# Kernel optimization log

Hardware: AMD Instinct MI355X
Metric: run time of the kernel (lower is better)

Reference implementation:

```python
import jax, jax.numpy as jnp
import numpy as np

B, T, C, H = 8, 1024, 1024, 16
D = C // H
EPS = 1e-5

def _ln(x, g, b):
    mu = jnp.mean(x, axis=-1, keepdims=True)
    var = jnp.var(x, axis=-1, keepdims=True)
    return (x - mu) * jax.lax.rsqrt(var + EPS) * g + b

def _build_mask(cond_mask, cond_len, token_len):
    # Vectorized form of the per-batch Python-loop mask in the torch module.
    counts = jnp.sum(cond_mask, axis=-1)            # [B] number of valid cond tokens
    rows = jnp.arange(T)
    cols = jnp.arange(T)
    # all rows may attend to the first counts[i] (cond) columns
    m_cond = cols[None, None, :] < counts[:, None, None]          # [B,1,T]
    m_cond = jnp.broadcast_to(m_cond, (B, T, T))
    # block-causal tiled pattern on rows/cols >= cond_len:
    # value = (col - cond_len) % token_len <= (row - cond_len) % token_len
    pattern = ((cols[None, :] - cond_len) % token_len) <= ((rows[:, None] - cond_len) % token_len)
    m_block = (rows[:, None] >= cond_len) & (cols[None, :] >= cond_len) & pattern  # [T,T]
    # cols >= cond_len: overwritten by block pattern (rows < cond_len stay 0 there)
    mask = jnp.where(cols[None, None, :] < cond_len, m_cond, m_block[None, :, :])
    return mask[:, None, :, :]                      # [B,1,T,T] bool

def _attn(x, Wq, bq, Wk, bk, Wv, bv, Wp, bp, cond_mask, cond_len, token_len):
    q = (x @ Wq + bq).reshape(B, T, H, D).transpose(0, 2, 1, 3)  # [B,H,T,D]
    k = (x @ Wk + bk).reshape(B, T, H, D).transpose(0, 2, 1, 3)
    v = (x @ Wv + bv).reshape(B, T, H, D).transpose(0, 2, 1, 3)
    att = jnp.einsum('bhqd,bhkd->bhqk', q, k) * (1.0 / np.sqrt(D))
    mask = _build_mask(cond_mask, cond_len, token_len)
    att = jnp.where(mask, att, -jnp.inf)
    att = jax.nn.softmax(att, axis=-1)
    y = jnp.einsum('bhqk,bhkd->bhqd', att, v)
    y = y.transpose(0, 2, 1, 3).reshape(B, T, C)
    return y @ Wp + bp

def setup_inputs() -> dict:
    key = jax.random.key(0)
    ks = jax.random.split(key, 16)
    cond_len, token_len = 256, 768
    s = 1.0 / np.sqrt(C)
    counts = jax.random.randint(ks[0], (B,), 1, cond_len + 1)
    cond_mask = (jnp.arange(T)[None, :] < counts[:, None]).astype(jnp.int32)
    return {
        'x': jax.random.normal(ks[1], (B, T, C), jnp.float32),
        'ln1_g': jnp.ones((C,), jnp.float32), 'ln1_b': jnp.zeros((C,), jnp.float32),
        'Wq': jax.random.normal(ks[2], (C, C), jnp.float32) * s, 'bq': jnp.zeros((C,), jnp.float32),
        'Wk': jax.random.normal(ks[3], (C, C), jnp.float32) * s, 'bk': jnp.zeros((C,), jnp.float32),
        'Wv': jax.random.normal(ks[4], (C, C), jnp.float32) * s, 'bv': jnp.zeros((C,), jnp.float32),
        'Wp': jax.random.normal(ks[5], (C, C), jnp.float32) * s, 'bp': jnp.zeros((C,), jnp.float32),
        'ln2_g': jnp.ones((C,), jnp.float32), 'ln2_b': jnp.zeros((C,), jnp.float32),
        'W1': jax.random.normal(ks[6], (C, 4 * C), jnp.float32) * s, 'b1': jnp.zeros((4 * C,), jnp.float32),
        'W2': jax.random.normal(ks[7], (4 * C, C), jnp.float32) * (0.5 * s), 'b2': jnp.zeros((C,), jnp.float32),
        'cond_mask': cond_mask,
        'cond_len': cond_len,
        'token_len': token_len,
    }

def reference(x, ln1_g, ln1_b, Wq, bq, Wk, bk, Wv, bv, Wp, bp, ln2_g, ln2_b, W1, b1, W2, b2, cond_mask, cond_len, token_len):
    x = x + _attn(_ln(x, ln1_g, ln1_b), Wq, bq, Wk, bk, Wv, bv, Wp, bp, cond_mask, cond_len, token_len)
    h = _ln(x, ln2_g, ln2_b)
    x = x + (jax.nn.gelu(h @ W1 + b1, approximate=False) @ W2 + b2)
    return x
```

## Files before the change

### kernel.cpp

```cpp
#include <hip/hip_runtime.h>
#include <hip/hip_bf16.h>
#include <cstdint>
#include <cstddef>

typedef __attribute__((ext_vector_type(8))) short short8;
typedef __attribute__((ext_vector_type(4))) float f32x4;
typedef __attribute__((ext_vector_type(4))) unsigned short us4;

#define MFMA_BF16(a, b, c) __builtin_amdgcn_mfma_f32_16x16x32_bf16((a), (b), (c), 0, 0, 0)
#define VMCNT(n) asm volatile("s_waitcnt vmcnt(" #n ")" ::: "memory")

__device__ __forceinline__ unsigned short f2bf(float f) {
  unsigned int u = __float_as_uint(f);
  u += 0x7FFFu + ((u >> 16) & 1u);
  return (unsigned short)(u >> 16);
}

__device__ __forceinline__ float gelu_fast(float v) {
  const float u = v * (0.79788456f + 0.03567741f * v * v);
  const float e = exp2f(u * 2.88539008f);
  return v - v * __builtin_amdgcn_rcpf(e + 1.0f);
}

typedef const void __attribute__((address_space(1)))* as1_cvp;
typedef void __attribute__((address_space(3)))* as3_vp;
__device__ __forceinline__ void gll16(const short* g, short* l) {
#if defined(__HIP_DEVICE_COMPILE__)
  __builtin_amdgcn_global_load_lds((as1_cvp)g, (as3_vp)l, 16, 0, 0);
#else
  (void)g; (void)l;
#endif
}

__global__ void prep_kernel(const int* __restrict__ cm, int* __restrict__ counts,
                            const float* __restrict__ bq, const float* __restrict__ bk,
                            const float* __restrict__ bv, float* __restrict__ dst) {
  const int t = threadIdx.x;
  if (blockIdx.x < 12) {
    const int i = blockIdx.x * 256 + t;
    dst[i] = (i < 1024) ? bq[i] : (i < 2048 ? bk[i - 1024] : bv[i - 2048]);
    return;
  }
  __shared__ int sd[256];
  const int b = blockIdx.x - 12;
  int s = 0;
  for (int i = t; i < 1024; i += 256) s += cm[b * 1024 + i];
  sd[t] = s; __syncthreads();
  for (int k = 128; k > 0; k >>= 1) { if (t < k) sd[t] += sd[t + k]; __syncthreads(); }
  if (t == 0) counts[b] = sd[0];
}

__global__ void transpose4_kernel(const float* __restrict__ Wq, const float* __restrict__ Wk,
                                  const float* __restrict__ Wv, const float* __restrict__ Wp,
                                  unsigned short* __restrict__ wqkvT,
                                  unsigned short* __restrict__ wpT) {
  __shared__ float tile[32][33];
  const int z = blockIdx.z;
  const float* src = (z == 0) ? Wq : (z == 1) ? Wk : (z == 2) ? Wv : Wp;
  unsigned short* dst = (z < 3) ? wqkvT + (size_t)z * 1024 * 1024 : wpT;
  const int c0 = blockIdx.x * 32, r0 = blockIdx.y * 32;
  const int tx = threadIdx.x, ty = threadIdx.y;
  #pragma unroll
  for (int i = ty; i < 32; i += 8)
    tile[i][tx] = src[(size_t)(r0 + i) * 1024 + (c0 + tx)];
  __syncthreads();
  #pragma unroll
  for (int i = ty; i < 32; i += 8)
    dst[(size_t)(c0 + i) * 1024 + (r0 + tx)] = f2bf(tile[tx][i]);
}

__global__ void transpose_kernel(const float* __restrict__ src, unsigned short* __restrict__ dst,
                                 int R, int C) {
  __shared__ float tile[32][33];
  const int c0 = blockIdx.x * 32, r0 = blockIdx.y * 32;
  const int tx = threadIdx.x, ty = threadIdx.y;
  #pragma unroll
  for (int i = ty; i < 32; i += 8)
    tile[i][tx] = src[(size_t)(r0 + i) * C + (c0 + tx)];
  __syncthreads();
  #pragma unroll
  for (int i = ty; i < 32; i += 8)
    dst[(size_t)(c0 + i) * R + (r0 + tx)] = f2bf(tile[tx][i]);
}

__global__ __launch_bounds__(256) void ln_kernel(const float* __restrict__ in,
                                                 const float* __restrict__ gw,
                                                 const float* __restrict__ bw,
                                                 unsigned short* __restrict__ out) {
  const int row = blockIdx.x, t = threadIdx.x;
  const float4 v = ((const float4*)(in + (size_t)row * 1024))[t];
  float s = v.x + v.y + v.z + v.w;
  float ss = v.x * v.x + v.y * v.y + v.z * v.z + v.w * v.w;
  #pragma unroll
  for (int o = 32; o >= 1; o >>= 1) { s += __shfl_down(s, o, 64); ss += __shfl_down(ss, o, 64); }
  __shared__ float red[8];
  if ((t & 63) == 0) { red[t >> 6] = s; red[4 + (t >> 6)] = ss; }
  __syncthreads();
  const float S  = red[0] + red[1] + red[2] + red[3];
  const float SS = red[4] + red[5] + red[6] + red[7];
  const float mu = S * (1.0f / 1024.0f);
  const float var = SS * (1.0f / 1024.0f) - mu * mu;
  const float rs = rsqrtf(var + 1e-5f);
  const int c = t * 4;
  const float4 g4 = ((const float4*)gw)[t];
  const float4 b4 = ((const float4*)bw)[t];
  us4 o4;
  o4[0] = f2bf((v.x - mu) * rs * g4.x + b4.x);
  o4[1] = f2bf((v.y - mu) * rs * g4.y + b4.y);
  o4[2] = f2bf((v.z - mu) * rs * g4.z + b4.z);
  o4[3] = f2bf((v.w - mu) * rs * g4.w + b4.w);
  *(us4*)(out + (size_t)row * 1024 + c) = o4;
}

__global__ __launch_bounds__(256) void red_kernel(
    const unsigned short* __restrict__ p0, const unsigned short* __restrict__ p1,
    const float* __restrict__ bias, const float* __restrict__ res,
    float* __restrict__ out) {
  const int i = (blockIdx.x * 256 + threadIdx.x) * 4;
  const us4 a = *(const us4*)(p0 + i);
  const us4 b = *(const us4*)(p1 + i);
  const float4 r = *(const float4*)(res + i);
  const float4 bv = *(const float4*)(bias + (i & 1023));
  float4 o;
  o.x = __uint_as_float((unsigned)a[0] << 16) + __uint_as_float((unsigned)b[0] << 16) + bv.x + r.x;
  o.y = __uint_as_float((unsigned)a[1] << 16) + __uint_as_float((unsigned)b[1] << 16) + bv.y + r.y;
  o.z = __uint_as_float((unsigned)a[2] << 16) + __uint_as_float((unsigned)b[2] << 16) + bv.z + r.z;
  o.w = __uint_as_float((unsigned)a[3] << 16) + __uint_as_float((unsigned)b[3] << 16) + bv.w + r.w;
  *(float4*)(out + i) = o;
}

template <int EPI>
__global__ __launch_bounds__(256, 2) void gemm128_kernel(
    const short* __restrict__ A, const short* __restrict__ BT,
    const float* __restrict__ bias, int N, int K, int kstr, int gm, int skoff,
    unsigned short* __restrict__ outb, unsigned short* __restrict__ outb2,
    unsigned short* __restrict__ outb3,
    float* __restrict__ outf, const float* __restrict__ res) {
  __shared__ alignas(16) short lds[36864];
  const int t = threadIdx.x;
  const int l = t & 63, w = t >> 6;
  const int lq = l & 15, g = l >> 4;
  const int wc = w;
  const int cpx = (int)gridDim.x >> 3;
  int wid = ((int)blockIdx.x & 7) * cpx + ((int)blockIdx.x >> 3);
  int slice = 0;
  if (EPI == 4) { slice = wid >> 8; wid &= 255; }
  const short* Ap = A + (size_t)slice * skoff;
  const short* Bp = BT + (size_t)slice * skoff;
  unsigned short* outp = (EPI == 4 && slice) ? outb2 : outb;
  const int bm = (wid % gm) * 128, bn = (wid / gm) * 256;
  const int NT = K >> 5;

  const int csw = ((t & 3) ^ ((t >> 3) & 3)) * 8;
  const int sr = t >> 2;

  const f32x4 z4 = {0.f, 0.f, 0.f, 0.f};
  f32x4 acc[8][4];
  #pragma unroll
  for (int i = 0; i < 8; i++)
    #pragma unroll
    for (int j = 0; j < 4; j++) acc[i][j] = z4;

  auto stageA = [&](int buf, int k0) {
    const short* src = Ap + (size_t)(bm + sr) * kstr + k0 + csw;
    short* dst = lds + buf * 12288 + t * 8;
    gll16(src, dst);
    gll16(src + (size_t)64 * kstr, dst + 2048);
  };
  auto stageB = [&](int buf, int k0) {
    const short* src = Bp + (size_t)(bn + sr) * kstr + k0 + csw;
    short* dst = lds + buf * 12288 + 4096 + t * 8;
    gll16(src, dst);
    gll16(src + (size_t)64 * kstr,  dst + 2048);
    gll16(src + (size_t)128 * kstr, dst + 4096);
    gll16(src + (size_t)192 * kstr, dst + 6144);
  };
  const int swu = (g ^ ((lq >> 1) & 3)) * 8;
  auto rdA = [&](int buf, int mi) {
    const int ra = mi * 16 + lq;
    return *(const short8*)(lds + buf * 12288 + ra * 32 + swu);
  };
  auto rdB = [&](int buf, int ni) {
    const int rb = wc * 64 + ni * 16 + lq;
    return *(const short8*)(lds + buf * 12288 + 4096 + rb * 32 + swu);
  };

  stageA(0, 0);  stageB(0, 0);
  stageA(1, 32); stageB(1, 32);
  VMCNT(6);
  __builtin_amdgcn_s_barrier();

  int cur = 0;
  for (int v = 0; v < NT; ++v) {
    const int nx1 = (cur == 2) ? 0 : cur + 1;
    const int nx2 = (nx1 == 2) ? 0 : nx1 + 1;
    short8 a[8], b[4];
    #pragma unroll
    for (int mi = 0; mi < 8; ++mi) a[mi] = rdA(cur, mi);
    #pragma unroll
    for (int ni = 0; ni < 4; ++ni) b[ni] = rdB(cur, ni);
    if (v + 2 < NT) {
      stageA(nx2, (v + 2) * 32); stageB(nx2, (v + 2) * 32);
      VMCNT(6);
    } else {
      VMCNT(0);
    }
    __builtin_amdgcn_s_barrier();
    __builtin_amdgcn_s_setprio(1);
    #pragma unroll
    for (int mi = 0; mi < 8; ++mi)
      #pragma unroll
      for (int ni = 0; ni < 4; ++ni)
        acc[mi][ni] = MFMA_BF16(a[mi], b[ni], acc[mi][ni]);
    __builtin_amdgcn_s_setprio(0);
    cur = nx1;
  }

  if (EPI == 2) {
    #pragma unroll
    for (int mi = 0; mi < 8; ++mi) {
      #pragma unroll
      for (int ni = 0; ni < 4; ++ni) {
        const int col = bn + wc * 64 + ni * 16 + lq;
        const float bv = bias[col];
        #pragma unroll
        for (int r = 0; r < 4; ++r) {
          const int row = bm + mi * 16 + 4 * g + r;
          const size_t idx = (size_t)row * N + col;
          outf[idx] = acc[mi][ni][r] + bv + res[idx];
        }
      }
    }
    return;
  }

  __syncthreads();
  const float qscale = (EPI == 3 && bn < 1024) ? 0.125f * 1.44269504088896f : 1.0f;
  unsigned short* eb = (unsigned short*)lds;
  #pragma unroll
  for (int mi = 0; mi < 8; ++mi) {
    #pragma unroll
    for (int ni = 0; ni < 4; ++ni) {
      const int col = wc * 64 + ni * 16 + lq;
      const float bv = (EPI == 4) ? 0.f : bias[bn + col];
      #pragma unroll
      for (int r = 0; r < 4; ++r) {
        const int row = mi * 16 + 4 * g + r;
        float vv = acc[mi][ni][r] + bv;
        if (EPI == 1) vv = gelu_fast(vv);
        if (EPI == 3) vv *= qscale;
        eb[row * 256 + col] = f2bf(vv);
      }
    }
  }
  __syncthreads();

  if (EPI == 3 && bn >= 1024 && bn < 2048) {
    const int bb = bm >> 10;
    #pragma unroll
    for (int it = 0; it < 16; ++it) {
      const int unit = it * 256 + t;
      const int row = unit >> 5, c8 = unit & 31;
      const int col = c8 * 8;
      const int hh = (bn - 1024 + col) >> 6;
      const int c = (col & 63) >> 3;
      const int tt = (bm + row) & 1023;
      const int ti = tt >> 5, kvr = tt & 31;
      const int lqk = ((kvr >> 3) << 2) | (kvr & 3);
      const int frag = (((kvr >> 2) & 1) << 1) | (c >> 2);
      const int lane = ((c & 3) << 4) | lqk;
      const short8 vv = *(const short8*)(lds + unit * 8);
      *(short8*)((short*)outb2 + ((size_t)(bb * 16 + hh) * 32 + ti) * 2048
                 + frag * 512 + lane * 8) = vv;
    }
    return;
  }
  if (EPI == 3 && bn >= 2048) {
    const int bb = bm >> 10;
    const int bt = (bm & 1023) >> 5;
    #pragma unroll
    for (int it = 0; it < 16; ++it) {
      const int u = it * 256 + t;
      const int s = u >> 8;
      const int til = s & 3, hl = s >> 2;
      const int fl = u & 255;
      const int dc = fl >> 6, lane = fl & 63;
      const int lqv = lane & 15, gv = lane >> 4;
      short8 vv;
      #pragma unroll
      for (int j = 0; j < 8; ++j)
        vv[j] = (short)eb[(til * 32 + 8 * gv + j) * 256 + hl * 64 + 16 * dc + lqv];
      const int hh = ((bn - 2048) >> 6) + hl;
      *(short8*)((short*)outb3 + ((size_t)(bb * 16 + hh) * 32 + (bt + til)) * 2048
                 + dc * 512 + lane * 8) = vv;
    }
    return;
  }

  #pragma unroll
  for (int it = 0; it < 16; ++it) {
    const int unit = it * 256 + t;
    const int row = unit >> 5, c8 = unit & 31;
    const short8 vv = *(const short8*)(lds + unit * 8);
    *(short8*)((short*)outp + (size_t)(bm + row) * N + bn + c8 * 8) = vv;
  }
}

__global__ __launch_bounds__(256) void attn_kernel(
    const short* __restrict__ qkv, const short* __restrict__ kp,
    const short* __restrict__ vp, unsigned short* __restrict__ y,
    const int* __restrict__ counts) {
  const int blk = blockIdx.x;
  const int slot = blk >> 3;
  const int pb = slot & 7;
  const int bh = ((slot >> 3) << 3) | (blk & 7);
  const int b = bh >> 4, h = bh & 15;
  const int w = threadIdx.x >> 6, l = threadIdx.x & 63;
  const int p = pb + 8 * w;
  const int lq = l & 15, g = l >> 4;
  const int qb0 = p * 16, qb1 = (63 - p) * 16;
  const int count = counts[b];

  const short* base  = qkv + (size_t)b * 1024 * 3072 + h * 64;
  const short* kbase = kp + (size_t)bh * 65536 + l * 8;
  const short* vbase = vp + (size_t)bh * 65536 + l * 8;

  short8 qf[2][2];
  {
    const short* qr0 = base + (size_t)(qb0 + lq) * 3072 + 8 * g;
    const short* qr1 = base + (size_t)(qb1 + lq) * 3072 + 8 * g;
    qf[0][0] = *(const short8*)qr0; qf[0][1] = *(const short8*)(qr0 + 32);
    qf[1][0] = *(const short8*)qr1; qf[1][1] = *(const short8*)(qr1 + 32);
  }

  const f32x4 z4 = {0.f, 0.f, 0.f, 0.f};
  f32x4 oacc[2][4];
  #pragma unroll
  for (int grp = 0; grp < 2; ++grp)
    #pragma unroll
    for (int dc = 0; dc < 4; ++dc) oacc[grp][dc] = z4;
  float mrun[2] = {-1e30f, -1e30f};
  float lrun[2] = {0.f, 0.f};
  const int ncond = min((count + 31) >> 5, 8);
  const int ncausal = (qb1 + 16 - 256 + 31) >> 5;
  const int nt = ncond + ncausal;
  auto kv_of = [&](int i) { return i < ncond ? i * 32 : 256 + (i - ncond) * 32; };

  auto loadt = [&](int kv0, short8 (&kr)[4], short8 (&vr)[4]) {
    const short* kpp = kbase + (size_t)(kv0 >> 5) * 2048;
    kr[0] = *(const short8*)kpp;
    kr[1] = *(const short8*)(kpp + 512);
    kr[2] = *(const short8*)(kpp + 1024);
    kr[3] = *(const short8*)(kpp + 1536);
    const short* vpp = vbase + (size_t)(kv0 >> 5) * 2048;
    #pragma unroll
    for (int dc = 0; dc < 4; ++dc)
      vr[dc] = *(const short8*)(vpp + dc * 512);
  };

  auto compute = [&](int i, const short8 (&kr)[4], const short8 (&vr)[4]) {
    const int kv0 = kv_of(i);
    const bool isCond = (i < ncond);
    #pragma unroll
    for (int grp = 0; grp < 2; ++grp) {
      const int qb = grp ? qb1 : qb0;
      if (!isCond && kv0 >= qb + 16) continue;
      const bool needMask = isCond ? (kv0 + 32 > count) : (kv0 + 31 > qb);
      f32x4 sA = z4, sB = z4;
      __builtin_amdgcn_s_setprio(1);
      sA = MFMA_BF16(kr[0], qf[grp][0], sA);
      sA = MFMA_BF16(kr[1], qf[grp][1], sA);
      sB = MFMA_BF16(kr[2], qf[grp][0], sB);
      sB = MFMA_BF16(kr[3], qf[grp][1], sB);
      __builtin_amdgcn_s_setprio(0);
      const int q = qb + lq;
      float mx = -1e30f;
      if (needMask) {
        #pragma unroll
        for (int r = 0; r < 4; ++r) {
          const int colA = kv0 + 8 * g + r, colB = colA + 4;
          const bool okA = isCond ? (colA < count) : (colA <= q);
          const bool okB = isCond ? (colB < count) : (colB <= q);
          const float vA = okA ? sA[r] : -1e30f;
          const float vB = okB ? sB[r] : -1e30f;
          sA[r] = vA; sB[r] = vB;
          mx = fmaxf(fmaxf(vA, vB), mx);
        }
      } else {
        #pragma unroll
        for (int r = 0; r < 4; ++r)
          mx = fmaxf(fmaxf(sA[r], sB[r]), mx);
      }
      mx = fmaxf(mx, __shfl_xor(mx, 16, 64));
      mx = fmaxf(mx, __shfl_xor(mx, 32, 64));
      float m = mrun[grp];
      if (!__all(mx <= m + 8.0f)) {
        const float mn = fmaxf(m, mx);
        const float sf = exp2f(m - mn);
        lrun[grp] *= sf;
        #pragma unroll
        for (int dc = 0; dc < 4; ++dc)
          #pragma unroll
          for (int r = 0; r < 4; ++r) oacc[grp][dc][r] *= sf;
        mrun[grp] = mn; m = mn;
      }
      float ps = 0.f;
      #pragma unroll
      for (int r = 0; r < 4; ++r) {
        const float aa = exp2f(sA[r] - m);
        const float c2 = exp2f(sB[r] - m);
        sA[r] = aa; sB[r] = c2; ps += aa + c2;
      }
      lrun[grp] += ps;
      union { short8 s8; __hip_bfloat162 h2[4]; } pu;
      pu.h2[0] = __float22bfloat162_rn(float2{sA[0], sA[1]});
      pu.h2[1] = __float22bfloat162_rn(float2{sA[2], sA[3]});
      pu.h2[2] = __float22bfloat162_rn(float2{sB[0], sB[1]});
      pu.h2[3] = __float22bfloat162_rn(float2{sB[2], sB[3]});
      __builtin_amdgcn_s_setprio(1);
      #pragma unroll
      for (int dc = 0; dc < 4; ++dc)
        oacc[grp][dc] = MFMA_BF16(vr[dc], pu.s8, oacc[grp][dc]);
      __builtin_amdgcn_s_setprio(0);
    }
  };

  short8 kb0[4], vb0[4], kb1[4], vb1[4];
  loadt(kv_of(0), kb0, vb0);
  for (int i = 0; i < nt; i += 2) {
    if (i + 1 < nt) loadt(kv_of(i + 1), kb1, vb1);
    compute(i, kb0, vb0);
    if (i + 1 >= nt) break;
    if (i + 2 < nt) loadt(kv_of(i + 2), kb0, vb0);
    compute(i + 1, kb1, vb1);
  }

  #pragma unroll
  for (int grp = 0; grp < 2; ++grp) {
    float ls = lrun[grp];
    ls += __shfl_xor(ls, 16, 64);
    ls += __shfl_xor(ls, 32, 64);
    const float inv = 1.0f / ls;
    const int qb = grp ? qb1 : qb0;
    unsigned short* yr = y + (size_t)(b * 1024 + qb + lq) * 1024 + h * 64;
    #pragma unroll
    for (int dc = 0; dc < 4; ++dc)
      #pragma unroll
      for (int r = 0; r < 4; ++r)
        yr[16 * dc + 4 * g + r] = f2bf(oacc[grp][dc][r] * inv);
  }
}

extern "C" void kernel_launch(void* const* d_in, const int* in_sizes, int n_in,
                              void* d_out, int out_size, void* d_ws, size_t ws_size,
                              hipStream_t stream) {
  (void)in_sizes; (void)n_in; (void)out_size; (void)ws_size;
  const float* x     = (const float*)d_in[0];
  const float* ln1_g = (const float*)d_in[1];
  const float* ln1_b = (const float*)d_in[2];
  const float* Wq    = (const float*)d_in[3];
  const float* bq    = (const float*)d_in[4];
  const float* Wk    = (const float*)d_in[5];
  const float* bk    = (const float*)d_in[6];
  const float* Wv    = (const float*)d_in[7];
  const float* bv    = (const float*)d_in[8];
  const float* Wp    = (const float*)d_in[9];
  const float* bp    = (const float*)d_in[10];
  const float* ln2_g = (const float*)d_in[11];
  const float* ln2_b = (const float*)d_in[12];
  const float* W1    = (const float*)d_in[13];
  const float* b1    = (const float*)d_in[14];
  const float* W2    = (const float*)d_in[15];
  const float* b2    = (const float*)d_in[16];
  const int* cond_mask = (const int*)d_in[17];

  char* ws = (char*)d_ws;
  const size_t MB = 1u << 20;
  short* xn    = (short*)(ws + 0);
  short* qkv   = (short*)(ws + 16 * MB);
  short* act   = (short*)(ws + 0);
  unsigned short* yb = (unsigned short*)(ws + 64 * MB);
  unsigned short* part0 = (unsigned short*)(ws + 64 * MB);
  short* kpack = (short*)(ws + 80 * MB);
  float* x1    = (float*)(ws + 80 * MB);
  short* vpack = (short*)(ws + 112 * MB);
  short* hb    = (short*)(ws + 112 * MB);
  unsigned short* part1 = (unsigned short*)(ws + 112 * MB);
  short* wqkvT = (short*)(ws + 128 * MB);
  short* wpT   = (short*)(ws + 134 * MB);
  short* w1T   = (short*)(ws + 136 * MB);
  short* w2T   = (short*)(ws + 144 * MB);
  float* bqkv  = (float*)(ws + 152 * MB);
  int* counts  = (int*)(ws + 152 * MB + 16384);

  const dim3 tb(32, 8);
  prep_kernel<<<20, 256, 0, stream>>>(cond_mask, counts, bq, bk, bv, bqkv);
  transpose4_kernel<<<dim3(32, 32, 4), tb, 0, stream>>>(Wq, Wk, Wv, Wp,
                                                        (unsigned short*)wqkvT,
                                                        (unsigned short*)wpT);
  transpose_kernel<<<dim3(128, 32), tb, 0, stream>>>(W1, (unsigned short*)w1T, 1024, 4096);
  transpose_kernel<<<dim3(32, 128), tb, 0, stream>>>(W2, (unsigned short*)w2T, 4096, 1024);
  ln_kernel<<<8192, 256, 0, stream>>>(x, ln1_g, ln1_b, (unsigned short*)xn);

  gemm128_kernel<3><<<768, 256, 0, stream>>>(xn, wqkvT, bqkv, 3072, 1024, 1024, 64, 0,
                                             (unsigned short*)qkv, (unsigned short*)kpack,
                                             (unsigned short*)vpack, nullptr, nullptr);
  attn_kernel<<<1024, 256, 0, stream>>>(qkv, kpack, vpack, yb, counts);
  gemm128_kernel<2><<<256, 256, 0, stream>>>((const short*)yb, wpT, bp, 1024, 1024, 1024, 64, 0,
                                             nullptr, nullptr, nullptr, x1, x);
  ln_kernel<<<8192, 256, 0, stream>>>(x1, ln2_g, ln2_b, (unsigned short*)hb);
  gemm128_kernel<1><<<1024, 256, 0, stream>>>(hb, w1T, b1, 4096, 1024, 1024, 64, 0,
                                              (unsigned short*)act, nullptr, nullptr,
                                              nullptr, nullptr);
  gemm128_kernel<4><<<512, 256, 0, stream>>>(act, w2T, nullptr, 1024, 2048, 4096, 64, 2048,
                                             part0, part1, nullptr, nullptr, nullptr);
  red_kernel<<<8192, 256, 0, stream>>>(part0, part1, b2, x1, (float*)d_out);
}
```

Measured before the change: 378.3 us.

## Shrink GEMM LDS to double buffer and split epilogue to raise occupancy

Changes the GEMM main loop from a triple-buffered LDS ring to double buffering, issuing the next-next tile's loads after the MFMA block behind two barriers. The epilogue is split into two 64-row halves so the staging buffer fits in the smaller LDS allocation. Launch bounds go from 2 to 3 blocks per CU. This trades load/compute overlap and an extra barrier per iteration for higher occupancy, and accumulator register pressure may limit how much the extra block helps.

Result: slower. 1.078 ms (+185.1%).

```diff
diff --git a/kernel.cpp b/kernel.cpp
--- a/kernel.cpp
+++ b/kernel.cpp
@@ -130,13 +130,13 @@
 }
 
 template <int EPI>
-__global__ __launch_bounds__(256, 2) void gemm128_kernel(
+__global__ __launch_bounds__(256, 3) void gemm128_kernel(
     const short* __restrict__ A, const short* __restrict__ BT,
     const float* __restrict__ bias, int N, int K, int kstr, int gm, int skoff,
     unsigned short* __restrict__ outb, unsigned short* __restrict__ outb2,
     unsigned short* __restrict__ outb3,
     float* __restrict__ outf, const float* __restrict__ res) {
-  __shared__ alignas(16) short lds[36864];
+  __shared__ alignas(16) short lds[24576];
   const int t = threadIdx.x;
   const int l = t & 63, w = t >> 6;
   const int lq = l & 15, g = l >> 4;
@@ -190,22 +190,13 @@
   VMCNT(6);
   __builtin_amdgcn_s_barrier();
 
-  int cur = 0;
   for (int v = 0; v < NT; ++v) {
-    const int nx1 = (cur == 2) ? 0 : cur + 1;
-    const int nx2 = (nx1 == 2) ? 0 : nx1 + 1;
+    const int cur = v & 1;
     short8 a[8], b[4];
     #pragma unroll
     for (int mi = 0; mi < 8; ++mi) a[mi] = rdA(cur, mi);
     #pragma unroll
     for (int ni = 0; ni < 4; ++ni) b[ni] = rdB(cur, ni);
-    if (v + 2 < NT) {
-      stageA(nx2, (v + 2) * 32); stageB(nx2, (v + 2) * 32);
-      VMCNT(6);
-    } else {
-      VMCNT(0);
-    }
-    __builtin_amdgcn_s_barrier();
     __builtin_amdgcn_s_setprio(1);
     #pragma unroll
     for (int mi = 0; mi < 8; ++mi)
@@ -213,7 +204,10 @@
       for (int ni = 0; ni < 4; ++ni)
         acc[mi][ni] = MFMA_BF16(a[mi], b[ni], acc[mi][ni]);
     __builtin_amdgcn_s_setprio(0);
-    cur = nx1;
+    __builtin_amdgcn_s_barrier();
+    if (v + 2 < NT) { stageA(cur, (v + 2) * 32); stageB(cur, (v + 2) * 32); }
+    if (v + 2 < NT) { VMCNT(6); } else { VMCNT(0); }
+    __builtin_amdgcn_s_barrier();
   }
 
   if (EPI == 2) {
@@ -234,75 +228,78 @@
     return;
   }
 
-  __syncthreads();
   const float qscale = (EPI == 3 && bn < 1024) ? 0.125f * 1.44269504088896f : 1.0f;
   unsigned short* eb = (unsigned short*)lds;
   #pragma unroll
-  for (int mi = 0; mi < 8; ++mi) {
-    #pragma unroll
-    for (int ni = 0; ni < 4; ++ni) {
-      const int col = wc * 64 + ni * 16 + lq;
-      const float bv = (EPI == 4) ? 0.f : bias[bn + col];
-      #pragma unroll
-      for (int r = 0; r < 4; ++r) {
-        const int row = mi * 16 + 4 * g + r;
-        float vv = acc[mi][ni][r] + bv;
-        if (EPI == 1) vv = gelu_fast(vv);
-        if (EPI == 3) vv *= qscale;
-        eb[row * 256 + col] = f2bf(vv);
+  for (int half = 0; half < 2; ++half) {
+    __syncthreads();
+    #pragma unroll
+    for (int mi2 = 0; mi2 < 4; ++mi2) {
+      const int mi = half * 4 + mi2;
+      #pragma unroll
+      for (int ni = 0; ni < 4; ++ni) {
+        const int col = wc * 64 + ni * 16 + lq;
+        const float bv = (EPI == 4) ? 0.f : bias[bn + col];
+        #pragma unroll
+        for (int r = 0; r < 4; ++r) {
+          const int relrow = mi2 * 16 + 4 * g + r;
+          float vv = acc[mi][ni][r] + bv;
+          if (EPI == 1) vv = gelu_fast(vv);
+          if (EPI == 3) vv *= qscale;
+          eb[relrow * 256 + col] = f2bf(vv);
+        }
       }
     }
-  }
-  __syncthreads();
-
-  if (EPI == 3 && bn >= 1024 && bn < 2048) {
-    const int bb = bm >> 10;
-    #pragma unroll
-    for (int it = 0; it < 16; ++it) {
-      const int unit = it * 256 + t;
-      const int row = unit >> 5, c8 = unit & 31;
-      const int col = c8 * 8;
-      const int hh = (bn - 1024 + col) >> 6;
-      const int c = (col & 63) >> 3;
-      const int tt = (bm + row) & 1023;
-      const int ti = tt >> 5, kvr = tt & 31;
-      const int lqk = ((kvr >> 3) << 2) | (kvr & 3);
-      const int frag = (((kvr >> 2) & 1) << 1) | (c >> 2);
-      const int lane = ((c & 3) << 4) | lqk;
-      const short8 vv = *(const short8*)(lds + unit * 8);
-      *(short8*)((short*)outb2 + ((size_t)(bb * 16 + hh) * 32 + ti) * 2048
-                 + frag * 512 + lane * 8) = vv;
+    __syncthreads();
+
+    if (EPI == 3 && bn >= 1024 && bn < 2048) {
+      const int bb = bm >> 10;
+      #pragma unroll
+      for (int it = 0; it < 8; ++it) {
+        const int unit = it * 256 + t;
+        const int relrow = unit >> 5, c8 = unit & 31;
+        const int col = c8 * 8;
+        const int hh = (bn - 1024 + col) >> 6;
+        const int c = (col & 63) >> 3;
+        const int tt = (bm + half * 64 + relrow) & 1023;
+        const int ti = tt >> 5, kvr = tt & 31;
+        const int lqk = ((kvr >> 3) << 2) | (kvr & 3);
+        const int frag = (((kvr >> 2) & 1) << 1) | (c >> 2);
+        const int lane = ((c & 3) << 4) | lqk;
+        const short8 vv = *(const short8*)(lds + unit * 8);
+        *(short8*)((short*)outb2 + ((size_t)(bb * 16 + hh) * 32 + ti) * 2048
+                   + frag * 512 + lane * 8) = vv;
+      }
+    } else if (EPI == 3 && bn >= 2048) {
+      const int bb = bm >> 10;
+      const int bt = (bm & 1023) >> 5;
+      #pragma unroll
+      for (int it = 0; it < 8; ++it) {
+        const int u = it * 256 + t;
+        const int s = u >> 8;
+        const int til_rel = s & 1, hl = s >> 1;
+        const int fl = u & 255;
+        const int dc = fl >> 6, lane = fl & 63;
+        const int lqv = lane & 15, gv = lane >> 4;
+        short8 vv;
+        #pragma unroll
+        for (int j = 0; j < 8; ++j)
+          vv[j] = (short)eb[(til_rel * 32 + 8 * gv + j) * 256 + hl * 64 + 16 * dc + lqv];
+        const int hh = ((bn - 2048) >> 6) + hl;
+        const int til_abs = half * 2 + til_rel;
+        *(short8*)((short*)outb3 + ((size_t)(bb * 16 + hh) * 32 + (bt + til_abs)) * 2048
+                   + dc * 512 + lane * 8) = vv;
+      }
+    } else {
+      #pragma unroll
+      for (int it = 0; it < 8; ++it) {
+        const int unit = it * 256 + t;
+        const int relrow = unit >> 5, c8 = unit & 31;
+        const int row = half * 64 + relrow;
+        const short8 vv = *(const short8*)(lds + unit * 8);
+        *(short8*)((short*)outp + (size_t)(bm + row) * N + bn + c8 * 8) = vv;
+      }
     }
-    return;
-  }
-  if (EPI == 3 && bn >= 2048) {
-    const int bb = bm >> 10;
-    const int bt = (bm & 1023) >> 5;
-    #pragma unroll
-    for (int it = 0; it < 16; ++it) {
-      const int u = it * 256 + t;
-      const int s = u >> 8;
-      const int til = s & 3, hl = s >> 2;
-      const int fl = u & 255;
-      const int dc = fl >> 6, lane = fl & 63;
-      const int lqv = lane & 15, gv = lane >> 4;
-      short8 vv;
-      #pragma unroll
-      for (int j = 0; j < 8; ++j)
-        vv[j] = (short)eb[(til * 32 + 8 * gv + j) * 256 + hl * 64 + 16 * dc + lqv];
-      const int hh = ((bn - 2048) >> 6) + hl;
-      *(short8*)((short*)outb3 + ((size_t)(bb * 16 + hh) * 32 + (bt + til)) * 2048
-                 + dc * 512 + lane * 8) = vv;
-    }
-    return;
-  }
-
-  #pragma unroll
-  for (int it = 0; it < 16; ++it) {
-    const int unit = it * 256 + t;
-    const int row = unit >> 5, c8 = unit & 31;
-    const short8 vv = *(const short8*)(lds + unit * 8);
-    *(short8*)((short*)outp + (size_t)(bm + row) * N + bn + c8 * 8) = vv;
   }
 }
 
```
